# Performance work log

Hardware: AMD Instinct MI355X
Metric: run time of the kernel (lower is better)

## Reference

```python
import jax, jax.numpy as jnp
import numpy as np

N_NODES = 100000


def _gcn_layer(x, src, dst, deg_inv_sqrt, W, b):
    # GCNConv: out = D^{-1/2} (A + I) D^{-1/2} X W + b  (symmetric norm, self-loops)
    xw = x @ W  # [N, out]
    norm = deg_inv_sqrt[src] * deg_inv_sqrt[dst]  # [E]
    msg = xw[src] * norm[:, None]  # [E, out] gathered messages
    agg = jax.ops.segment_sum(msg, dst, num_segments=N_NODES)
    # self-loop contribution: norm_ii = deg_inv_sqrt[i]^2
    agg = agg + (deg_inv_sqrt * deg_inv_sqrt)[:, None] * xw
    return agg + b


def setup_inputs() -> dict:
    key = jax.random.key(0)
    k1, k2, k3, k4, k5, k6 = jax.random.split(key, 6)
    F_IN, HID, OUT, E = 128, 256, 40, 1600000
    x = jax.random.normal(k1, (N_NODES, F_IN), dtype=jnp.float32)
    edge_index = jax.random.randint(k2, (2, E), 0, N_NODES, dtype=jnp.int64)
    s1 = 1.0 / np.sqrt(F_IN)
    s2 = 1.0 / np.sqrt(HID)
    W1 = jax.random.uniform(k3, (F_IN, HID), jnp.float32, -s1, s1)
    b1 = jnp.zeros((HID,), jnp.float32)
    W2 = jax.random.uniform(k4, (HID, OUT), jnp.float32, -s2, s2)
    b2 = jnp.zeros((OUT,), jnp.float32)
    return {"x": x, "edge_index": edge_index, "W1": W1, "b1": b1, "W2": W2, "b2": b2}


def reference(x, edge_index, W1, b1, W2, b2):
    src, dst = edge_index[0], edge_index[1]
    # degree with self-loops (GCNConv default add_self_loops=True)
    deg = jax.ops.segment_sum(jnp.ones_like(dst, dtype=x.dtype), dst, num_segments=N_NODES) + 1.0
    deg_inv_sqrt = jax.lax.rsqrt(deg)
    h = _gcn_layer(x, src, dst, deg_inv_sqrt, W1, b1)
    h = jax.nn.relu(h)
    # dropout is identity in eval mode
    h = _gcn_layer(h, src, dst, deg_inv_sqrt, W2, b2)
    return jax.nn.log_softmax(h, axis=1)
```

## Files before the change

kernel.cpp:

```cpp
#include <hip/hip_runtime.h>
#include <math.h>

typedef long long ll;
typedef unsigned int uint;
typedef __attribute__((ext_vector_type(8))) short bf16x8;
typedef __attribute__((ext_vector_type(4))) float f32x4;

#define FIN 128
#define HID 256
#define FOUT 40
#define NG 8
#define NBIN 64
#define CAPPAD 65536

__device__ __forceinline__ float bflo(uint u) { return __uint_as_float(u << 16); }
__device__ __forceinline__ float bfhi(uint u) { return __uint_as_float(u & 0xFFFF0000u); }
__device__ __forceinline__ unsigned short f2bf(float f) {
  uint u = __float_as_uint(f);
  u += 0x7FFFu + ((u >> 16) & 1u);
  return (unsigned short)(u >> 16);
}

__device__ __forceinline__ int detect64(const uint* __restrict__ ei) {
  return (ei[1] == 0u && ei[3] == 0u && ei[5] == 0u && ei[7] == 0u) ? 1 : 0;
}

__global__ __launch_bounds__(256) void k_init(
    const void* __restrict__ ei,
    const float* __restrict__ W1, const float* __restrict__ W2,
    unsigned short* __restrict__ w1p, unsigned short* __restrict__ w2p,
    int2* __restrict__ partbuf, int* __restrict__ pcur,
    ll E, int range, ll cap) {
  __shared__ int wrun[4][NG], wbase[4][NG], lbase[NG];
  int t = threadIdx.x;
  int i = blockIdx.x * 256 + t;
  int lane = t & 63, w = t >> 6;

  if (i < 32768) {
    int j = i & 7, g = (i >> 3) & 3, c = (i >> 5) & 255, s = i >> 13;
    int k = s * 32 + g * 8 + j;
    w1p[i] = f2bf(W1[(size_t)k * HID + c]);
  } else if (i < 32768 + 12288) {
    int i2 = i - 32768;
    int j = i2 & 7, g = (i2 >> 3) & 3, q = i2 >> 5;
    int c = q % 48, s = q / 48;
    int k = s * 32 + g * 8 + j;
    w2p[i2] = (c < FOUT) ? f2bf(W2[(size_t)k * FOUT + c]) : (unsigned short)0;
  }

  int is64 = detect64((const uint*)ei);
  ll base = (ll)i * 4;
  int m = 0;
  int s[4], d[4], p[4] = {-1, -1, -1, -1};
  if (base < E) {
    m = (int)((E - base < 4) ? (E - base) : 4);
    if (is64) {
      if (m == 4) {
        longlong2 a0 = *(const longlong2*)((const ll*)ei + base);
        longlong2 a1 = *(const longlong2*)((const ll*)ei + base + 2);
        longlong2 b0 = *(const longlong2*)((const ll*)ei + E + base);
        longlong2 b1 = *(const longlong2*)((const ll*)ei + E + base + 2);
        s[0]=(int)a0.x; s[1]=(int)a0.y; s[2]=(int)a1.x; s[3]=(int)a1.y;
        d[0]=(int)b0.x; d[1]=(int)b0.y; d[2]=(int)b1.x; d[3]=(int)b1.y;
      } else {
        for (int j = 0; j < m; ++j) { s[j]=(int)((const ll*)ei)[base+j]; d[j]=(int)((const ll*)ei)[E+base+j]; }
      }
    } else {
      if (m == 4) {
        int4 a = *(const int4*)((const int*)ei + base);
        int4 b = *(const int4*)((const int*)ei + E + base);
        s[0]=a.x; s[1]=a.y; s[2]=a.z; s[3]=a.w;
        d[0]=b.x; d[1]=b.y; d[2]=b.z; d[3]=b.w;
      } else {
        for (int j = 0; j < m; ++j) { s[j]=((const int*)ei)[base+j]; d[j]=((const int*)ei)[E+base+j]; }
      }
    }
    for (int j = 0; j < m; ++j) p[j] = d[j] / range;
  }

  int run[NG] = {0,0,0,0,0,0,0,0};
  int rank[4] = {0,0,0,0};
  unsigned long long lt = (1ull << lane) - 1ull;
  #pragma unroll
  for (int j = 0; j < 4; ++j) {
    #pragma unroll
    for (int g = 0; g < NG; ++g) {
      unsigned long long mm = __ballot(p[j] == g);
      if (p[j] == g) rank[j] = run[g] + (int)__popcll(mm & lt);
      run[g] += (int)__popcll(mm);
    }
  }
  if (lane < NG) wrun[w][lane] = run[lane];
  __syncthreads();
  if (t < NG) {
    int acc = 0;
    for (int ww = 0; ww < 4; ++ww) { wbase[ww][t] = acc; acc += wrun[ww][t]; }
    lbase[t] = acc ? atomicAdd(&pcur[t], acc) : 0;
  }
  __syncthreads();
  for (int j = 0; j < m; ++j) {
    int g = p[j];
    ll slot = (ll)lbase[g] + wbase[w][g] + rank[j];
    if (slot < cap) partbuf[(ll)g * cap + slot] = make_int2(s[j], d[j]);
  }
}

__global__ __launch_bounds__(256) void k_count(
    const int2* __restrict__ partbuf, const int* __restrict__ pcur,
    int* __restrict__ cnt, ll cap) {
  int g = blockIdx.x & (NG - 1);
  const int2* pb = partbuf + (ll)g * cap;
  int cnt_g = min(pcur[g], (int)cap);
  int bg = blockIdx.x >> 3, NB = gridDim.x >> 3;
  for (int i = bg * 256 + threadIdx.x; i < cnt_g; i += NB * 256) {
    int2 p = pb[i];
    atomicAdd(&cnt[p.y], 1);
  }
}

__global__ __launch_bounds__(1024) void k_scan1(const int* __restrict__ cnt,
                                                int* __restrict__ row_off,
                                                int* __restrict__ blksums, int n) {
  __shared__ int sm[1024];
  int t = threadIdx.x;
  int base = blockIdx.x * 4096 + t * 4;
  int v0 = (base + 0 < n) ? cnt[base + 0] : 0;
  int v1 = (base + 1 < n) ? cnt[base + 1] : 0;
  int v2 = (base + 2 < n) ? cnt[base + 2] : 0;
  int v3 = (base + 3 < n) ? cnt[base + 3] : 0;
  int s = v0 + v1 + v2 + v3;
  sm[t] = s;
  __syncthreads();
  for (int off = 1; off < 1024; off <<= 1) {
    int u = (t >= off) ? sm[t - off] : 0;
    __syncthreads();
    sm[t] += u;
    __syncthreads();
  }
  int excl = sm[t] - s;
  if (base + 0 < n) row_off[base + 0] = excl;
  if (base + 1 < n) row_off[base + 1] = excl + v0;
  if (base + 2 < n) row_off[base + 2] = excl + v0 + v1;
  if (base + 3 < n) row_off[base + 3] = excl + v0 + v1 + v2;
  if (t == 1023) blksums[blockIdx.x] = sm[1023];
}

__global__ void k_scan2(int* __restrict__ blksums, int nb) {
  if (threadIdx.x == 0 && blockIdx.x == 0) {
    int acc = 0;
    for (int i = 0; i < nb; ++i) { int v = blksums[i]; blksums[i] = acc; acc += v; }
    blksums[nb] = acc;
  }
}

__global__ __launch_bounds__(1024) void k_scan3(
    int* __restrict__ row_off, int* __restrict__ cursor,
    const int* __restrict__ blksums, float* __restrict__ dis,
    int* __restrict__ hist, int n, int nb) {
  __shared__ int lh[NBIN];
  int t = threadIdx.x;
  if (t < NBIN) lh[t] = 0;
  __syncthreads();
  int i = blockIdx.x * 1024 + t;
  if (i < n) {
    int c = cursor[i];
    int v = row_off[i] + blksums[i >> 12];
    row_off[i] = v;
    cursor[i] = v;
    dis[i] = rsqrtf((float)c + 1.0f);
    atomicAdd(&lh[min(c, NBIN - 1)], 1);
  }
  if (i == 0) row_off[n] = blksums[nb];
  __syncthreads();
  if (t < NBIN && lh[t]) atomicAdd(&hist[t], lh[t]);
}

__global__ __launch_bounds__(256) void k_perm(
    const int* __restrict__ row_off, const int* __restrict__ hist,
    int* __restrict__ pbincur, int* __restrict__ perm, int n) {
  __shared__ int lh[NBIN], lbase[NBIN], pfx[NBIN];
  int t = threadIdx.x;
  if (t < NBIN) { lh[t] = 0; pfx[t] = hist[t]; }
  __syncthreads();
  if (t == 0) {
    int acc = 0;
    for (int b = 0; b < NBIN; ++b) { int v = pfx[b]; pfx[b] = acc; acc += v; }
  }
  int base = blockIdx.x * 4096 + t * 16;
  int deg[16];
  #pragma unroll
  for (int j = 0; j < 16; ++j) {
    int i = base + j;
    if (i < n) {
      deg[j] = min(row_off[i + 1] - row_off[i], NBIN - 1);
      atomicAdd(&lh[deg[j]], 1);
    } else deg[j] = -1;
  }
  __syncthreads();
  if (t < NBIN) {
    lbase[t] = pfx[t] + (lh[t] ? atomicAdd(&pbincur[t], lh[t]) : 0);
    lh[t] = 0;
  }
  __syncthreads();
  #pragma unroll
  for (int j = 0; j < 16; ++j) {
    if (deg[j] >= 0) {
      int r = atomicAdd(&lh[deg[j]], 1);
      perm[lbase[deg[j]] + r] = base + j;
    }
  }
}

__global__ __launch_bounds__(256) void k_fill(
    const int2* __restrict__ partbuf, const int* __restrict__ pcur,
    int* __restrict__ cursor, int* __restrict__ csr, ll cap) {
  int g = blockIdx.x & (NG - 1);
  const int2* pb = partbuf + (ll)g * cap;
  int cnt_g = min(pcur[g], (int)cap);
  int bg = blockIdx.x >> 3, NB = gridDim.x >> 3;
  for (int i = bg * 256 + threadIdx.x; i < cnt_g; i += NB * 256) {
    int2 p = pb[i];
    int pos = atomicAdd(&cursor[p.y], 1);
    csr[pos] = p.x;
  }
}

__global__ __launch_bounds__(256) void k_xcast(
    const float* __restrict__ x, const float* __restrict__ dis,
    unsigned short* __restrict__ xb, int total8) {
  int i = blockIdx.x * 256 + threadIdx.x;
  if (i >= total8) return;
  float w = dis[i >> 4];
  const float4* p = (const float4*)x + (size_t)i * 2;
  float4 a = p[0], b = p[1];
  uint4 o;
  o.x = (uint)f2bf(w * a.x) | ((uint)f2bf(w * a.y) << 16);
  o.y = (uint)f2bf(w * a.z) | ((uint)f2bf(w * a.w) << 16);
  o.z = (uint)f2bf(w * b.x) | ((uint)f2bf(w * b.y) << 16);
  o.w = (uint)f2bf(w * b.z) | ((uint)f2bf(w * b.w) << 16);
  *(uint4*)(xb + (size_t)i * 8) = o;
}

__device__ __forceinline__ void add8(float* a, uint4 r) {
  a[0] += bflo(r.x); a[1] += bfhi(r.x);
  a[2] += bflo(r.y); a[3] += bfhi(r.y);
  a[4] += bflo(r.z); a[5] += bfhi(r.z);
  a[6] += bflo(r.w); a[7] += bfhi(r.w);
}

__global__ __launch_bounds__(256) void k_fused1(
    const unsigned short* __restrict__ xb, const int* __restrict__ csr,
    const int* __restrict__ row_off, const float* __restrict__ dis,
    const int* __restrict__ perm,
    const unsigned short* __restrict__ w1p, const float* __restrict__ b1,
    const unsigned short* __restrict__ w2p, unsigned short* __restrict__ xw2b,
    int n)
{
  __shared__ __align__(16) unsigned short xsb[16 * 136];
  __shared__ __align__(16) unsigned short hsb[16 * 264];
  __shared__ int   nid[16];
  __shared__ float dsh[16];

  int tid = threadIdx.x;
  int n0 = blockIdx.x * 16;
  int wv = tid >> 6, lane = tid & 63, qq = lane >> 4, l16 = lane & 15;
  int nl = wv * 4 + qq;
  int idx = n0 + nl;
  int node = (idx < n) ? perm[idx] : -1;

  float a[8] = {0, 0, 0, 0, 0, 0, 0, 0};
  float di = 0.f;
  if (node >= 0) {
    di = dis[node];
    uint4 v = *((const uint4*)(xb + (size_t)node * FIN) + l16);
    add8(a, v);
    int e0 = row_off[node], e1 = row_off[node + 1];
    int e = e0;
    for (; e + 8 <= e1; e += 8) {
      int s0 = csr[e],     s1 = csr[e + 1], s2 = csr[e + 2], s3 = csr[e + 3];
      int s4 = csr[e + 4], s5 = csr[e + 5], s6 = csr[e + 6], s7 = csr[e + 7];
      uint4 r0 = *((const uint4*)(xb + (size_t)s0 * FIN) + l16);
      uint4 r1 = *((const uint4*)(xb + (size_t)s1 * FIN) + l16);
      uint4 r2 = *((const uint4*)(xb + (size_t)s2 * FIN) + l16);
      uint4 r3 = *((const uint4*)(xb + (size_t)s3 * FIN) + l16);
      uint4 r4 = *((const uint4*)(xb + (size_t)s4 * FIN) + l16);
      uint4 r5 = *((const uint4*)(xb + (size_t)s5 * FIN) + l16);
      uint4 r6 = *((const uint4*)(xb + (size_t)s6 * FIN) + l16);
      uint4 r7 = *((const uint4*)(xb + (size_t)s7 * FIN) + l16);
      add8(a, r0); add8(a, r1); add8(a, r2); add8(a, r3);
      add8(a, r4); add8(a, r5); add8(a, r6); add8(a, r7);
    }
    for (; e < e1; ++e) {
      uint4 r0 = *((const uint4*)(xb + (size_t)csr[e] * FIN) + l16);
      add8(a, r0);
    }
  }
  if (l16 == 0) { nid[nl] = node; dsh[nl] = di; }
  {
    uint4 pk;
    pk.x = (uint)f2bf(di * a[0]) | ((uint)f2bf(di * a[1]) << 16);
    pk.y = (uint)f2bf(di * a[2]) | ((uint)f2bf(di * a[3]) << 16);
    pk.z = (uint)f2bf(di * a[4]) | ((uint)f2bf(di * a[5]) << 16);
    pk.w = (uint)f2bf(di * a[6]) | ((uint)f2bf(di * a[7]) << 16);
    *(uint4*)(xsb + nl * 136 + l16 * 8) = pk;
  }
  __syncthreads();

  int mrow = lane & 15, g = lane >> 4;
  f32x4 acc1[4] = {{0,0,0,0},{0,0,0,0},{0,0,0,0},{0,0,0,0}};
  #pragma unroll
  for (int s = 0; s < 4; ++s) {
    bf16x8 av = *(const bf16x8*)(xsb + mrow * 136 + s * 32 + g * 8);
    #pragma unroll
    for (int t = 0; t < 4; ++t) {
      int c = wv * 64 + t * 16 + mrow;
      bf16x8 bv = *(const bf16x8*)(w1p + (((size_t)(s * 256 + c) * 4 + g) << 3));
      acc1[t] = __builtin_amdgcn_mfma_f32_16x16x32_bf16(av, bv, acc1[t], 0, 0, 0);
    }
  }
  #pragma unroll
  for (int t = 0; t < 4; ++t) {
    int c = wv * 64 + t * 16 + mrow;
    float bb = b1[c];
    #pragma unroll
    for (int r = 0; r < 4; ++r) {
      float v = fmaxf(acc1[t][r] + bb, 0.f);
      hsb[(g * 4 + r) * 264 + c] = f2bf(v);
    }
  }
  __syncthreads();

  if (wv < 3) {
    f32x4 acc2 = {0, 0, 0, 0};
    int c2 = wv * 16 + mrow;
    #pragma unroll
    for (int s = 0; s < 8; ++s) {
      bf16x8 av = *(const bf16x8*)(hsb + mrow * 264 + s * 32 + g * 8);
      bf16x8 bv = *(const bf16x8*)(w2p + (((size_t)(s * 48 + c2) * 4 + g) << 3));
      acc2 = __builtin_amdgcn_mfma_f32_16x16x32_bf16(av, bv, acc2, 0, 0, 0);
    }
    if (c2 < FOUT) {
      #pragma unroll
      for (int r = 0; r < 4; ++r) {
        int nodeg = nid[g * 4 + r];
        if (nodeg >= 0)
          xw2b[(size_t)nodeg * FOUT + c2] = f2bf(acc2[r] * dsh[g * 4 + r]);
      }
    }
  }
}

__global__ __launch_bounds__(256) void k_layer2(
    const unsigned short* __restrict__ xw2b, const int* __restrict__ csr,
    const int* __restrict__ row_off, const float* __restrict__ dis,
    const int* __restrict__ perm,
    const float* __restrict__ b2, float* __restrict__ out, int n)
{
  int tid = threadIdx.x;
  int idx = blockIdx.x * 16 + (tid >> 4);
  int l16 = tid & 15;
  if (idx >= n) return;
  int node = perm[idx];
  float di = dis[node];
  bool act = (l16 < 10);
  float a0 = 0.f, a1 = 0.f, a2 = 0.f, a3 = 0.f;
  if (act) {
    uint2 v = *((const uint2*)(xw2b + (size_t)node * FOUT) + l16);
    a0 = bflo(v.x); a1 = bfhi(v.x); a2 = bflo(v.y); a3 = bfhi(v.y);
  }
  int e0 = row_off[node], e1 = row_off[node + 1];
  int e = e0;
  for (; e + 8 <= e1; e += 8) {
    int s0 = csr[e],     s1 = csr[e + 1], s2 = csr[e + 2], s3 = csr[e + 3];
    int s4 = csr[e + 4], s5 = csr[e + 5], s6 = csr[e + 6], s7 = csr[e + 7];
    if (act) {
      uint2 r0 = *((const uint2*)(xw2b + (size_t)s0 * FOUT) + l16);
      uint2 r1 = *((const uint2*)(xw2b + (size_t)s1 * FOUT) + l16);
      uint2 r2 = *((const uint2*)(xw2b + (size_t)s2 * FOUT) + l16);
      uint2 r3 = *((const uint2*)(xw2b + (size_t)s3 * FOUT) + l16);
      uint2 r4 = *((const uint2*)(xw2b + (size_t)s4 * FOUT) + l16);
      uint2 r5 = *((const uint2*)(xw2b + (size_t)s5 * FOUT) + l16);
      uint2 r6 = *((const uint2*)(xw2b + (size_t)s6 * FOUT) + l16);
      uint2 r7 = *((const uint2*)(xw2b + (size_t)s7 * FOUT) + l16);
      a0 += bflo(r0.x); a1 += bfhi(r0.x); a2 += bflo(r0.y); a3 += bfhi(r0.y);
      a0 += bflo(r1.x); a1 += bfhi(r1.x); a2 += bflo(r1.y); a3 += bfhi(r1.y);
      a0 += bflo(r2.x); a1 += bfhi(r2.x); a2 += bflo(r2.y); a3 += bfhi(r2.y);
      a0 += bflo(r3.x); a1 += bfhi(r3.x); a2 += bflo(r3.y); a3 += bfhi(r3.y);
      a0 += bflo(r4.x); a1 += bfhi(r4.x); a2 += bflo(r4.y); a3 += bfhi(r4.y);
      a0 += bflo(r5.x); a1 += bfhi(r5.x); a2 += bflo(r5.y); a3 += bfhi(r5.y);
      a0 += bflo(r6.x); a1 += bfhi(r6.x); a2 += bflo(r6.y); a3 += bfhi(r6.y);
      a0 += bflo(r7.x); a1 += bfhi(r7.x); a2 += bflo(r7.y); a3 += bfhi(r7.y);
    }
  }
  for (; e < e1; ++e) {
    int s0 = csr[e];
    if (act) {
      uint2 r0 = *((const uint2*)(xw2b + (size_t)s0 * FOUT) + l16);
      a0 += bflo(r0.x); a1 += bfhi(r0.x); a2 += bflo(r0.y); a3 += bfhi(r0.y);
    }
  }
  float l0 = -INFINITY, l1 = -INFINITY, l2 = -INFINITY, l3 = -INFINITY;
  if (act) {
    float4 bv = *(const float4*)(b2 + l16 * 4);
    l0 = di * a0 + bv.x; l1 = di * a1 + bv.y;
    l2 = di * a2 + bv.z; l3 = di * a3 + bv.w;
  }
  float m = fmaxf(fmaxf(l0, l1), fmaxf(l2, l3));
  #pragma unroll
  for (int off = 8; off > 0; off >>= 1) m = fmaxf(m, __shfl_xor(m, off));
  float s = 0.f;
  if (act) s = expf(l0 - m) + expf(l1 - m) + expf(l2 - m) + expf(l3 - m);
  #pragma unroll
  for (int off = 8; off > 0; off >>= 1) s += __shfl_xor(s, off);
  if (act) {
    float ls = m + logf(s);
    float4 o = make_float4(l0 - ls, l1 - ls, l2 - ls, l3 - ls);
    *(float4*)(out + (size_t)node * FOUT + l16 * 4) = o;
  }
}

extern "C" void kernel_launch(void* const* d_in, const int* in_sizes, int n_in,
                              void* d_out, int out_size, void* d_ws, size_t ws_size,
                              hipStream_t stream) {
  const float* x  = (const float*)d_in[0];
  const void*  ei = d_in[1];
  const float* W1 = (const float*)d_in[2];
  const float* b1 = (const float*)d_in[3];
  const float* W2 = (const float*)d_in[4];
  const float* b2 = (const float*)d_in[5];
  float* out = (float*)d_out;

  int n = in_sizes[0] / FIN;
  ll  E = (ll)in_sizes[1] / 2;
  int nb = (n + 4095) / 4096;
  int range = (n + NG - 1) / NG;
  ll  cap = E / NG + CAPPAD;

  char* ws = (char*)d_ws;
  size_t off = 0;
  auto carve = [&](size_t bytes) -> char* {
    char* p = ws + off;
    off = (off + bytes + 255) & ~(size_t)255;
    return p;
  };
  int zn = n + NBIN + NBIN + NG;
  int*   zbase   = (int*)carve((size_t)zn * 4);
  int*   cursor  = zbase;
  int*   hist    = zbase + n;
  int*   pbincur = zbase + n + NBIN;
  int*   pcur    = zbase + n + NBIN + NBIN;
  int*   row_off = (int*)carve((size_t)(n + 1) * 4);
  int2*  partbuf = (int2*)carve((size_t)NG * cap * 8);
  int*   csr     = (int*)carve((size_t)E * 4);
  int*   blksums = (int*)carve(64 * 4);
  int*   perm    = (int*)carve((size_t)n * 4);
  float* dis     = (float*)carve((size_t)n * 4);
  unsigned short* xb   = (unsigned short*)carve((size_t)n * FIN * 2);
  unsigned short* w1p  = (unsigned short*)carve(32768 * 2);
  unsigned short* w2p  = (unsigned short*)carve(12288 * 2);
  unsigned short* xw2b = (unsigned short*)carve((size_t)n * FOUT * 2);
  (void)n_in; (void)out_size; (void)ws_size;

  int gx8   = (n * FIN / 8 + 255) / 256;
  int gt16  = (n + 15) / 16;
  int gperm = (n + 4095) / 4096;
  int ginit = (int)((E + 1023) / 1024);

  hipMemsetAsync(zbase, 0, (size_t)zn * 4, stream);

  hipLaunchKernelGGL(k_init,  dim3(ginit), dim3(256), 0, stream,
                     ei, W1, W2, w1p, w2p, partbuf, pcur, E, range, cap);
  hipLaunchKernelGGL(k_count, dim3(2048), dim3(256), 0, stream, partbuf, pcur, cursor, cap);
  hipLaunchKernelGGL(k_scan1, dim3(nb), dim3(1024), 0, stream, cursor, row_off, blksums, n);
  hipLaunchKernelGGL(k_scan2, dim3(1), dim3(1), 0, stream, blksums, nb);
  hipLaunchKernelGGL(k_scan3, dim3((n + 1023) / 1024), dim3(1024), 0, stream,
                     row_off, cursor, blksums, dis, hist, n, nb);
  hipLaunchKernelGGL(k_perm,  dim3(gperm), dim3(256), 0, stream,
                     row_off, hist, pbincur, perm, n);
  hipLaunchKernelGGL(k_fill,  dim3(2048), dim3(256), 0, stream, partbuf, pcur, cursor, csr, cap);
  hipLaunchKernelGGL(k_xcast, dim3(gx8), dim3(256), 0, stream, x, dis, xb, n * FIN / 8);
  hipLaunchKernelGGL(k_fused1, dim3(gt16), dim3(256), 0, stream,
                     xb, csr, row_off, dis, perm, w1p, b1, w2p, xw2b, n);
  hipLaunchKernelGGL(k_layer2, dim3(gt16), dim3(256), 0, stream,
                     xw2b, csr, row_off, dis, perm, b2, out, n);
}
```

Before: 312.9 us.

## Merge scan and fill/perm kernels, interleave tile order, unroll edge tails

Removes the single-thread k_scan2 launch by having every k_scan3 block recompute the block prefix in shared memory. It also merges k_perm and k_fill into one launch with a block-index split. The two aggregation kernels now visit tiles in a coprime-stride permuted order, which mixes high- and low-degree tiles across the GPU. Their remainder edge loops become a single 8-wide gather with clamped indices and zeroed lanes. This cuts launch count and tail latency, but adds redundant loads for short remainders and a serial prefix done by thread 0 of every scan3 block.

```diff
diff --git a/kernel.cpp b/kernel.cpp
--- a/kernel.cpp
+++ b/kernel.cpp
@@ -12,6 +12,7 @@
 #define NG 8
 #define NBIN 64
 #define CAPPAD 65536
+#define PERMBLKS 32
 
 __device__ __forceinline__ float bflo(uint u) { return __uint_as_float(u << 16); }
 __device__ __forceinline__ float bfhi(uint u) { return __uint_as_float(u & 0xFFFF0000u); }
@@ -142,15 +143,7 @@
   if (base + 1 < n) row_off[base + 1] = excl + v0;
   if (base + 2 < n) row_off[base + 2] = excl + v0 + v1;
   if (base + 3 < n) row_off[base + 3] = excl + v0 + v1 + v2;
-  if (t == 1023) blksums[blockIdx.x] = sm[1023];
-}
-
-__global__ void k_scan2(int* __restrict__ blksums, int nb) {
-  if (threadIdx.x == 0 && blockIdx.x == 0) {
-    int acc = 0;
-    for (int i = 0; i < nb; ++i) { int v = blksums[i]; blksums[i] = acc; acc += v; }
-    blksums[nb] = acc;
-  }
+  if (t == 1023) blksums[blockIdx.x] = s ? sm[1023] : sm[1023];
 }
 
 __global__ __launch_bounds__(1024) void k_scan3(
@@ -158,70 +151,77 @@
     const int* __restrict__ blksums, float* __restrict__ dis,
     int* __restrict__ hist, int n, int nb) {
   __shared__ int lh[NBIN];
+  __shared__ int bpfx[256];
   int t = threadIdx.x;
   if (t < NBIN) lh[t] = 0;
+  if (t == 0) {
+    int acc = 0;
+    for (int b = 0; b < nb; ++b) { bpfx[b] = acc; acc += blksums[b]; }
+    bpfx[nb] = acc;
+  }
   __syncthreads();
   int i = blockIdx.x * 1024 + t;
   if (i < n) {
     int c = cursor[i];
-    int v = row_off[i] + blksums[i >> 12];
+    int v = row_off[i] + bpfx[i >> 12];
     row_off[i] = v;
     cursor[i] = v;
     dis[i] = rsqrtf((float)c + 1.0f);
     atomicAdd(&lh[min(c, NBIN - 1)], 1);
   }
-  if (i == 0) row_off[n] = blksums[nb];
+  if (i == 0) row_off[n] = bpfx[nb];
   __syncthreads();
   if (t < NBIN && lh[t]) atomicAdd(&hist[t], lh[t]);
 }
 
-__global__ __launch_bounds__(256) void k_perm(
+__global__ __launch_bounds__(256) void k_fillperm(
+    const int2* __restrict__ partbuf, const int* __restrict__ pcur,
+    int* __restrict__ cursor, int* __restrict__ csr, ll cap,
     const int* __restrict__ row_off, const int* __restrict__ hist,
     int* __restrict__ pbincur, int* __restrict__ perm, int n) {
-  __shared__ int lh[NBIN], lbase[NBIN], pfx[NBIN];
   int t = threadIdx.x;
-  if (t < NBIN) { lh[t] = 0; pfx[t] = hist[t]; }
-  __syncthreads();
-  if (t == 0) {
-    int acc = 0;
-    for (int b = 0; b < NBIN; ++b) { int v = pfx[b]; pfx[b] = acc; acc += v; }
-  }
-  int base = blockIdx.x * 4096 + t * 16;
-  int deg[16];
-  #pragma unroll
-  for (int j = 0; j < 16; ++j) {
-    int i = base + j;
-    if (i < n) {
-      deg[j] = min(row_off[i + 1] - row_off[i], NBIN - 1);
-      atomicAdd(&lh[deg[j]], 1);
-    } else deg[j] = -1;
-  }
-  __syncthreads();
-  if (t < NBIN) {
-    lbase[t] = pfx[t] + (lh[t] ? atomicAdd(&pbincur[t], lh[t]) : 0);
-    lh[t] = 0;
-  }
-  __syncthreads();
-  #pragma unroll
-  for (int j = 0; j < 16; ++j) {
-    if (deg[j] >= 0) {
-      int r = atomicAdd(&lh[deg[j]], 1);
-      perm[lbase[deg[j]] + r] = base + j;
-    }
-  }
-}
-
-__global__ __launch_bounds__(256) void k_fill(
-    const int2* __restrict__ partbuf, const int* __restrict__ pcur,
-    int* __restrict__ cursor, int* __restrict__ csr, ll cap) {
-  int g = blockIdx.x & (NG - 1);
-  const int2* pb = partbuf + (ll)g * cap;
-  int cnt_g = min(pcur[g], (int)cap);
-  int bg = blockIdx.x >> 3, NB = gridDim.x >> 3;
-  for (int i = bg * 256 + threadIdx.x; i < cnt_g; i += NB * 256) {
-    int2 p = pb[i];
-    int pos = atomicAdd(&cursor[p.y], 1);
-    csr[pos] = p.x;
+  if (blockIdx.x < PERMBLKS) {
+    __shared__ int lh[NBIN], lbase[NBIN], pfx[NBIN];
+    if (t < NBIN) { lh[t] = 0; pfx[t] = hist[t]; }
+    __syncthreads();
+    if (t == 0) {
+      int acc = 0;
+      for (int b = 0; b < NBIN; ++b) { int v = pfx[b]; pfx[b] = acc; acc += v; }
+    }
+    int base = blockIdx.x * 4096 + t * 16;
+    int deg[16];
+    #pragma unroll
+    for (int j = 0; j < 16; ++j) {
+      int i = base + j;
+      if (i < n) {
+        deg[j] = min(row_off[i + 1] - row_off[i], NBIN - 1);
+        atomicAdd(&lh[deg[j]], 1);
+      } else deg[j] = -1;
+    }
+    __syncthreads();
+    if (t < NBIN) {
+      lbase[t] = pfx[t] + (lh[t] ? atomicAdd(&pbincur[t], lh[t]) : 0);
+      lh[t] = 0;
+    }
+    __syncthreads();
+    #pragma unroll
+    for (int j = 0; j < 16; ++j) {
+      if (deg[j] >= 0) {
+        int r = atomicAdd(&lh[deg[j]], 1);
+        perm[lbase[deg[j]] + r] = base + j;
+      }
+    }
+  } else {
+    int bid = blockIdx.x - PERMBLKS;
+    int g = blockIdx.x & (NG - 1);
+    const int2* pb = partbuf + (ll)g * cap;
+    int cnt_g = min(pcur[g], (int)cap);
+    int bg = bid >> 3, NB = (gridDim.x - PERMBLKS) >> 3;
+    for (int i = bg * 256 + t; i < cnt_g; i += NB * 256) {
+      int2 p = pb[i];
+      int pos = atomicAdd(&cursor[p.y], 1);
+      csr[pos] = p.x;
+    }
   }
 }
 
@@ -254,7 +254,7 @@
     const int* __restrict__ perm,
     const unsigned short* __restrict__ w1p, const float* __restrict__ b1,
     const unsigned short* __restrict__ w2p, unsigned short* __restrict__ xw2b,
-    int n)
+    int n, int ntiles, int stride)
 {
   __shared__ __align__(16) unsigned short xsb[16 * 136];
   __shared__ __align__(16) unsigned short hsb[16 * 264];
@@ -262,7 +262,8 @@
   __shared__ float dsh[16];
 
   int tid = threadIdx.x;
-  int n0 = blockIdx.x * 16;
+  int tile = (int)(((ll)blockIdx.x * stride) % ntiles);
+  int n0 = tile * 16;
   int wv = tid >> 6, lane = tid & 63, qq = lane >> 4, l16 = lane & 15;
   int nl = wv * 4 + qq;
   int idx = n0 + nl;
@@ -290,9 +291,31 @@
       add8(a, r0); add8(a, r1); add8(a, r2); add8(a, r3);
       add8(a, r4); add8(a, r5); add8(a, r6); add8(a, r7);
     }
-    for (; e < e1; ++e) {
-      uint4 r0 = *((const uint4*)(xb + (size_t)csr[e] * FIN) + l16);
-      add8(a, r0);
+    if (e < e1) {
+      int last = e1 - 1;
+      int s0 = csr[e];
+      int s1 = csr[min(e + 1, last)], s2 = csr[min(e + 2, last)];
+      int s3 = csr[min(e + 3, last)], s4 = csr[min(e + 4, last)];
+      int s5 = csr[min(e + 5, last)], s6 = csr[min(e + 6, last)];
+      int s7 = csr[min(e + 7, last)];
+      uint4 r0 = *((const uint4*)(xb + (size_t)s0 * FIN) + l16);
+      uint4 r1 = *((const uint4*)(xb + (size_t)s1 * FIN) + l16);
+      uint4 r2 = *((const uint4*)(xb + (size_t)s2 * FIN) + l16);
+      uint4 r3 = *((const uint4*)(xb + (size_t)s3 * FIN) + l16);
+      uint4 r4 = *((const uint4*)(xb + (size_t)s4 * FIN) + l16);
+      uint4 r5 = *((const uint4*)(xb + (size_t)s5 * FIN) + l16);
+      uint4 r6 = *((const uint4*)(xb + (size_t)s6 * FIN) + l16);
+      uint4 r7 = *((const uint4*)(xb + (size_t)s7 * FIN) + l16);
+      uint4 z = make_uint4(0, 0, 0, 0);
+      if (e + 1 > last) r1 = z;
+      if (e + 2 > last) r2 = z;
+      if (e + 3 > last) r3 = z;
+      if (e + 4 > last) r4 = z;
+      if (e + 5 > last) r5 = z;
+      if (e + 6 > last) r6 = z;
+      if (e + 7 > last) r7 = z;
+      add8(a, r0); add8(a, r1); add8(a, r2); add8(a, r3);
+      add8(a, r4); add8(a, r5); add8(a, r6); add8(a, r7);
     }
   }
   if (l16 == 0) { nid[nl] = node; dsh[nl] = di; }
@@ -354,10 +377,12 @@
     const unsigned short* __restrict__ xw2b, const int* __restrict__ csr,
     const int* __restrict__ row_off, const float* __restrict__ dis,
     const int* __restrict__ perm,
-    const float* __restrict__ b2, float* __restrict__ out, int n)
+    const float* __restrict__ b2, float* __restrict__ out,
+    int n, int ntiles, int stride)
 {
   int tid = threadIdx.x;
-  int idx = blockIdx.x * 16 + (tid >> 4);
+  int tile = (int)(((ll)blockIdx.x * stride) % ntiles);
+  int idx = tile * 16 + (tid >> 4);
   int l16 = tid & 15;
   if (idx >= n) return;
   int node = perm[idx];
@@ -392,11 +417,38 @@
       a0 += bflo(r7.x); a1 += bfhi(r7.x); a2 += bflo(r7.y); a3 += bfhi(r7.y);
     }
   }
-  for (; e < e1; ++e) {
+  if (e < e1) {
+    int last = e1 - 1;
     int s0 = csr[e];
+    int s1 = csr[min(e + 1, last)], s2 = csr[min(e + 2, last)];
+    int s3 = csr[min(e + 3, last)], s4 = csr[min(e + 4, last)];
+    int s5 = csr[min(e + 5, last)], s6 = csr[min(e + 6, last)];
+    int s7 = csr[min(e + 7, last)];
     if (act) {
+      uint2 z = make_uint2(0, 0);
       uint2 r0 = *((const uint2*)(xw2b + (size_t)s0 * FOUT) + l16);
+      uint2 r1 = *((const uint2*)(xw2b + (size_t)s1 * FOUT) + l16);
+      uint2 r2 = *((const uint2*)(xw2b + (size_t)s2 * FOUT) + l16);
+      uint2 r3 = *((const uint2*)(xw2b + (size_t)s3 * FOUT) + l16);
+      uint2 r4 = *((const uint2*)(xw2b + (size_t)s4 * FOUT) + l16);
+      uint2 r5 = *((const uint2*)(xw2b + (size_t)s5 * FOUT) + l16);
+      uint2 r6 = *((const uint2*)(xw2b + (size_t)s6 * FOUT) + l16);
+      uint2 r7 = *((const uint2*)(xw2b + (size_t)s7 * FOUT) + l16);
+      if (e + 1 > last) r1 = z;
+      if (e + 2 > last) r2 = z;
+      if (e + 3 > last) r3 = z;
+      if (e + 4 > last) r4 = z;
+      if (e + 5 > last) r5 = z;
+      if (e + 6 > last) r6 = z;
+      if (e + 7 > last) r7 = z;
       a0 += bflo(r0.x); a1 += bfhi(r0.x); a2 += bflo(r0.y); a3 += bfhi(r0.y);
+      a0 += bflo(r1.x); a1 += bfhi(r1.x); a2 += bflo(r1.y); a3 += bfhi(r1.y);
+      a0 += bflo(r2.x); a1 += bfhi(r2.x); a2 += bflo(r2.y); a3 += bfhi(r2.y);
+      a0 += bflo(r3.x); a1 += bfhi(r3.x); a2 += bflo(r3.y); a3 += bfhi(r3.y);
+      a0 += bflo(r4.x); a1 += bfhi(r4.x); a2 += bflo(r4.y); a3 += bfhi(r4.y);
+      a0 += bflo(r5.x); a1 += bfhi(r5.x); a2 += bflo(r5.y); a3 += bfhi(r5.y);
+      a0 += bflo(r6.x); a1 += bfhi(r6.x); a2 += bflo(r6.y); a3 += bfhi(r6.y);
+      a0 += bflo(r7.x); a1 += bfhi(r7.x); a2 += bflo(r7.y); a3 += bfhi(r7.y);
     }
   }
   float l0 = -INFINITY, l1 = -INFINITY, l2 = -INFINITY, l3 = -INFINITY;
@@ -435,6 +487,14 @@
   int nb = (n + 4095) / 4096;
   int range = (n + NG - 1) / NG;
   ll  cap = E / NG + CAPPAD;
+
+  int ntiles = (n + 15) / 16;
+  int stride = 1;
+  for (int c = (ntiles * 2 / 5) | 1; c < ntiles; c += 2) {
+    int a = c, b = ntiles;
+    while (b) { int r = a % b; a = b; b = r; }
+    if (a == 1) { stride = c; break; }
+  }
 
   char* ws = (char*)d_ws;
   size_t off = 0;
@@ -452,7 +512,7 @@
   int*   row_off = (int*)carve((size_t)(n + 1) * 4);
   int2*  partbuf = (int2*)carve((size_t)NG * cap * 8);
   int*   csr     = (int*)carve((size_t)E * 4);
-  int*   blksums = (int*)carve(64 * 4);
+  int*   blksums = (int*)carve(256 * 4);
   int*   perm    = (int*)carve((size_t)n * 4);
   float* dis     = (float*)carve((size_t)n * 4);
   unsigned short* xb   = (unsigned short*)carve((size_t)n * FIN * 2);
@@ -462,8 +522,6 @@
   (void)n_in; (void)out_size; (void)ws_size;
 
   int gx8   = (n * FIN / 8 + 255) / 256;
-  int gt16  = (n + 15) / 16;
-  int gperm = (n + 4095) / 4096;
   int ginit = (int)((E + 1023) / 1024);
 
   hipMemsetAsync(zbase, 0, (size_t)zn * 4, stream);
@@ -472,15 +530,13 @@
                      ei, W1, W2, w1p, w2p, partbuf, pcur, E, range, cap);
   hipLaunchKernelGGL(k_count, dim3(2048), dim3(256), 0, stream, partbuf, pcur, cursor, cap);
   hipLaunchKernelGGL(k_scan1, dim3(nb), dim3(1024), 0, stream, cursor, row_off, blksums, n);
-  hipLaunchKernelGGL(k_scan2, dim3(1), dim3(1), 0, stream, blksums, nb);
   hipLaunchKernelGGL(k_scan3, dim3((n + 1023) / 1024), dim3(1024), 0, stream,
                      row_off, cursor, blksums, dis, hist, n, nb);
-  hipLaunchKernelGGL(k_perm,  dim3(gperm), dim3(256), 0, stream,
-                     row_off, hist, pbincur, perm, n);
-  hipLaunchKernelGGL(k_fill,  dim3(2048), dim3(256), 0, stream, partbuf, pcur, cursor, csr, cap);
+  hipLaunchKernelGGL(k_fillperm, dim3(2048 + PERMBLKS), dim3(256), 0, stream,
+                     partbuf, pcur, cursor, csr, cap, row_off, hist, pbincur, perm, n);
   hipLaunchKernelGGL(k_xcast, dim3(gx8), dim3(256), 0, stream, x, dis, xb, n * FIN / 8);
-  hipLaunchKernelGGL(k_fused1, dim3(gt16), dim3(256), 0, stream,
-                     xb, csr, row_off, dis, perm, w1p, b1, w2p, xw2b, n);
-  hipLaunchKernelGGL(k_layer2, dim3(gt16), dim3(256), 0, stream,
-                     xw2b, csr, row_off, dis, perm, b2, out, n);
-}
+  hipLaunchKernelGGL(k_fused1, dim3(ntiles), dim3(256), 0, stream,
+                     xb, csr, row_off, dis, perm, w1p, b1, w2p, xw2b, n, ntiles, stride);
+  hipLaunchKernelGGL(k_layer2, dim3(ntiles), dim3(256), 0, stream,
+                     xw2b, csr, row_off, dis, perm, b2, out, n, ntiles, stride);
+}
```

Measured after the change: 296.1 us. -5.4%, faster.
